# Optimization experiments

Hardware: AMD Instinct MI355X
Metric: run time of the kernel (lower is better)

The kernel has to match this reference:

```python
import jax, jax.numpy as jnp
import numpy as np
import math

B, T, C, H = 2, 2048, 1024, 16
HD = C // H

def setup_inputs() -> dict:
    key = jax.random.key(0)
    ks = jax.random.split(key, 5)
    s_in = 1.0 / math.sqrt(C)
    x = jax.random.normal(ks[0], (B, T, C), dtype=jnp.float32)
    W_attn = jax.random.normal(ks[1], (C, 3 * C), dtype=jnp.float32) * s_in
    b_attn = jnp.zeros((3 * C,), dtype=jnp.float32)
    W_proj = jax.random.normal(ks[2], (C, C), dtype=jnp.float32) * s_in
    b_proj = jnp.zeros((C,), dtype=jnp.float32)
    return {"x": x, "W_attn": W_attn, "b_attn": b_attn, "W_proj": W_proj, "b_proj": b_proj}

def reference(x, W_attn, b_attn, W_proj, b_proj):
    Bx, Tx, Cx = x.shape
    c = x @ W_attn + b_attn  # [B,T,3C]
    q, k, v = jnp.split(c, 3, axis=2)
    # [B,T,H,hd] -> [B,H,T,hd]
    q = q.reshape(Bx, Tx, H, HD).transpose(0, 2, 1, 3)
    k = k.reshape(Bx, Tx, H, HD).transpose(0, 2, 1, 3)
    v = v.reshape(Bx, Tx, H, HD).transpose(0, 2, 1, 3)
    # NOTE: module scales by 1/sqrt(C), not 1/sqrt(head_dim)
    attn = jnp.einsum('bhqd,bhkd->bhqk', q, k) * (1.0 / math.sqrt(Cx))
    causal = jnp.tril(jnp.ones((Tx, Tx), dtype=bool))
    attn = jnp.where(causal[None, None], attn, -jnp.inf)
    attn = jax.nn.softmax(attn, axis=-1)
    y = jnp.einsum('bhqk,bhkd->bhqd', attn, v)
    y = y.transpose(0, 2, 1, 3).reshape(Bx, Tx, Cx)
    return y @ W_proj + b_proj
```

## Files before the change

kernel.cpp:

```cpp
#include <hip/hip_runtime.h>
#include <math.h>

#define Bv 2
#define Tv 2048
#define Cv 1024
#define Hv 16
#define HDv 64
#define Mv (Bv * Tv)
#define SZv (Bv * Hv * Tv * HDv)

typedef short bf16x8 __attribute__((ext_vector_type(8)));
typedef float f32x4 __attribute__((ext_vector_type(4)));

static __device__ __forceinline__ unsigned short f2bf(float f) {
    unsigned u = __float_as_uint(f);
    u += 0x7fffu + ((u >> 16) & 1u);
    return (unsigned short)(u >> 16);
}

static __device__ __forceinline__ unsigned f2bf2(float a, float b) {
    unsigned r;
    asm("v_cvt_pk_bf16_f32 %0, %1, %2" : "=v"(r) : "v"(a), "v"(b));
    return r;
}

#define AS1 __attribute__((address_space(1)))
#define AS3 __attribute__((address_space(3)))
#define GLD16(gp, lp) __builtin_amdgcn_global_load_lds( \
    (AS1 const void*)(const void*)(gp), (AS3 void*)(void*)(lp), 16, 0, 0)

__global__ __launch_bounds__(256) void cvt_kernel(
    const float* __restrict__ src, unsigned short* __restrict__ dst, int n4)
{
    int i = blockIdx.x * 256 + threadIdx.x;
    if (i < n4) {
        float4 f = ((const float4*)src)[i];
        ushort4 u;
        u.x = f2bf(f.x); u.y = f2bf(f.y); u.z = f2bf(f.z); u.w = f2bf(f.w);
        ((ushort4*)dst)[i] = u;
    }
}

__global__ __launch_bounds__(256) void transpose_kernel(
    const float* __restrict__ src, unsigned short* __restrict__ dst,
    int R, int Ncols)
{
    __shared__ float tile[32][33];
    const int c0 = blockIdx.x * 32, r0 = blockIdx.y * 32;
    const int tx = threadIdx.x & 31, ty = threadIdx.x >> 5;
    #pragma unroll
    for (int i = 0; i < 4; ++i)
        tile[ty + i * 8][tx] = src[(size_t)(r0 + ty + i * 8) * Ncols + c0 + tx];
    __syncthreads();
    #pragma unroll
    for (int i = 0; i < 4; ++i)
        dst[(size_t)(c0 + ty + i * 8) * R + r0 + tx] = f2bf(tile[tx][ty + i * 8]);
}

__device__ __forceinline__ void mm_mainloop_1024(
    const unsigned short* __restrict__ A, const unsigned short* __restrict__ Bt,
    unsigned short* AsLds, unsigned short* BsLds,
    int rowBase, int colBase, f32x4 acc[4][4])
{
    const int tid  = threadIdx.x;
    const int lane = tid & 63;
    const int w    = tid >> 6;
    const int quad = lane >> 4, l15 = lane & 15;
    const int wm = (w >> 1) * 64, wn = (w & 1) * 64;
    const int K = 1024;

    const int g0 = (w * 2 + 0) * 64 + lane;
    const int g1 = (w * 2 + 1) * 64 + lane;
    const int r0 = g0 >> 2, r1 = g1 >> 2;
    const int kc0 = (g0 & 3) ^ ((r0 >> 1) & 3);
    const int kc1 = (g1 & 3) ^ ((r1 >> 1) & 3);
    const size_t offA0 = (size_t)(rowBase + r0) * K + kc0 * 8;
    const size_t offA1 = (size_t)(rowBase + r1) * K + kc1 * 8;
    const size_t offB0 = (size_t)(colBase + r0) * K + kc0 * 8;
    const size_t offB1 = (size_t)(colBase + r1) * K + kc1 * 8;
    unsigned short* ldsA0 = AsLds + (size_t)(w * 2 + 0) * 64 * 8;
    unsigned short* ldsA1 = AsLds + (size_t)(w * 2 + 1) * 64 * 8;
    unsigned short* ldsB0 = BsLds + (size_t)(w * 2 + 0) * 64 * 8;
    unsigned short* ldsB1 = BsLds + (size_t)(w * 2 + 1) * 64 * 8;

    const int sw = quad ^ ((l15 >> 1) & 3);
    int aoff[4], boff[4];
    #pragma unroll
    for (int i = 0; i < 4; ++i) {
        aoff[i] = ((wm + i * 16 + l15) * 4 + sw) * 8;
        boff[i] = ((wn + i * 16 + l15) * 4 + sw) * 8;
    }

    for (int k0 = 0; k0 < K; k0 += 32) {
        GLD16(A + offA0 + k0, ldsA0);
        GLD16(A + offA1 + k0, ldsA1);
        GLD16(Bt + offB0 + k0, ldsB0);
        GLD16(Bt + offB1 + k0, ldsB1);
        asm volatile("s_waitcnt vmcnt(0)" ::: "memory");
        __syncthreads();

        bf16x8 a[4], b[4];
        #pragma unroll
        for (int i = 0; i < 4; ++i) a[i] = *(const bf16x8*)(AsLds + aoff[i]);
        #pragma unroll
        for (int i = 0; i < 4; ++i) b[i] = *(const bf16x8*)(BsLds + boff[i]);

        #pragma unroll
        for (int mi = 0; mi < 4; ++mi)
            #pragma unroll
            for (int ni = 0; ni < 4; ++ni)
                acc[mi][ni] = __builtin_amdgcn_mfma_f32_16x16x32_bf16(
                    a[mi], b[ni], acc[mi][ni], 0, 0, 0);
        __syncthreads();
    }
}

__global__ __launch_bounds__(256) void qkv_mm_kernel(
    const unsigned short* __restrict__ xB, const unsigned short* __restrict__ WaT,
    const float* __restrict__ bias,
    unsigned short* __restrict__ qB, unsigned short* __restrict__ kB,
    unsigned short* __restrict__ vT)
{
    __shared__ __align__(16) unsigned short lds[128 * 136];
    const int rowBase = blockIdx.y * 128;
    const int colBase = blockIdx.x * 128;

    f32x4 acc[4][4];
    #pragma unroll
    for (int i = 0; i < 4; ++i)
        #pragma unroll
        for (int j = 0; j < 4; ++j) acc[i][j] = (f32x4){0.f, 0.f, 0.f, 0.f};

    mm_mainloop_1024(xB, WaT, lds, lds + 4096, rowBase, colBase, acc);

    const int tid = threadIdx.x, lane = tid & 63, w = tid >> 6;
    const int quad = lane >> 4, l15 = lane & 15;
    const int wm = (w >> 1) * 64, wn = (w & 1) * 64;
    const int s = colBase / Cv;
    const int tloc = rowBase & (Tv - 1);
    const int bh0 = (rowBase / Tv) * Hv + (colBase % Cv) / HDv;

    if (s < 2) {
        const float qs = (s == 0) ? 0.04508422f : 1.0f;
        #pragma unroll
        for (int mi = 0; mi < 4; ++mi)
            #pragma unroll
            for (int ni = 0; ni < 4; ++ni) {
                float bv = bias[colBase + wn + ni * 16 + l15];
                #pragma unroll
                for (int r = 0; r < 4; ++r) {
                    int m = wm + mi * 16 + quad * 4 + r;
                    int n = wn + ni * 16 + l15;
                    lds[m * 136 + n] = f2bf((acc[mi][ni][r] + bv) * qs);
                }
            }
        __syncthreads();
        unsigned short* dst = (s == 0) ? qB : kB;
        #pragma unroll
        for (int it = 0; it < 8; ++it) {
            int cc = tid + it * 256;
            int m = cc >> 4, j = cc & 15;
            uint4 v = *(const uint4*)(lds + m * 136 + j * 8);
            int hh = j >> 3, d0 = (j & 7) * 8;
            *(uint4*)(dst + ((size_t)(bh0 + hh) * Tv + tloc + m) * HDv + d0) = v;
        }
    } else {
        #pragma unroll
        for (int mi = 0; mi < 4; ++mi)
            #pragma unroll
            for (int ni = 0; ni < 4; ++ni) {
                float bv = bias[colBase + wn + ni * 16 + l15];
                #pragma unroll
                for (int r = 0; r < 4; ++r) {
                    int m = wm + mi * 16 + quad * 4 + r;
                    int n = wn + ni * 16 + l15;
                    lds[n * 136 + m] = f2bf(acc[mi][ni][r] + bv);
                }
            }
        __syncthreads();
        #pragma unroll
        for (int it = 0; it < 8; ++it) {
            int cc = tid + it * 256;
            int n = cc >> 4, j = cc & 15;
            uint4 v = *(const uint4*)(lds + n * 136 + j * 8);
            int hh = n >> 6, d = n & 63;
            *(uint4*)(vT + ((size_t)(bh0 + hh) * HDv + d) * Tv + tloc + j * 8) = v;
        }
    }
}

__global__ __launch_bounds__(256) void proj_mm_kernel(
    const unsigned short* __restrict__ y0B, const unsigned short* __restrict__ WpT,
    const float* __restrict__ bias, float* __restrict__ out)
{
    __shared__ __align__(16) unsigned short lds[8192];
    const int rowBase = blockIdx.y * 128;
    const int colBase = blockIdx.x * 128;

    f32x4 acc[4][4];
    #pragma unroll
    for (int i = 0; i < 4; ++i)
        #pragma unroll
        for (int j = 0; j < 4; ++j) acc[i][j] = (f32x4){0.f, 0.f, 0.f, 0.f};

    mm_mainloop_1024(y0B, WpT, lds, lds + 4096, rowBase, colBase, acc);

    const int tid = threadIdx.x, lane = tid & 63, w = tid >> 6;
    const int quad = lane >> 4, l15 = lane & 15;
    const int wm = (w >> 1) * 64, wn = (w & 1) * 64;

    #pragma unroll
    for (int mi = 0; mi < 4; ++mi)
        #pragma unroll
        for (int ni = 0; ni < 4; ++ni) {
            int n = colBase + wn + ni * 16 + l15;
            float bv = bias[n];
            #pragma unroll
            for (int r = 0; r < 4; ++r) {
                int m = rowBase + wm + mi * 16 + quad * 4 + r;
                out[(size_t)m * Cv + n] = acc[mi][ni][r] + bv;
            }
        }
}

__global__ __launch_bounds__(256) void attn_kernel(
    const unsigned short* __restrict__ qB, const unsigned short* __restrict__ kB,
    const unsigned short* __restrict__ vT, unsigned short* __restrict__ y0B)
{
    __shared__ __align__(16) unsigned short kv[1024 * 8];
    __shared__ __align__(16) unsigned short Pb[4][16 * 72];

    const int tid  = threadIdx.x;
    const int lane = tid & 63;
    const int w    = tid >> 6;
    const int quad = lane >> 4;
    const int l15  = lane & 15;

    const int qt = 31 - (blockIdx.x >> 5);
    const int bh = blockIdx.x & 31;
    const int qwbase = qt * 64 + w * 16;

    const unsigned short* qrow = qB + ((size_t)bh * Tv + qwbase + l15) * HDv;
    const bf16x8 Qa0 = *(const bf16x8*)(qrow + quad * 8);
    const bf16x8 Qa1 = *(const bf16x8*)(qrow + 32 + quad * 8);

    f32x4 O[4];
    float l[4] = {0.f, 0.f, 0.f, 0.f};
    #pragma unroll
    for (int n = 0; n < 4; ++n) O[n] = (f32x4){0.f, 0.f, 0.f, 0.f};

    const unsigned short* Kbase = kB + (size_t)bh * Tv * HDv;
    const unsigned short* Vbase = vT + (size_t)bh * HDv * Tv;
    unsigned short* Pw = &Pb[w][0];

    const unsigned short* gK[2];
    unsigned short* dK[2];
    #pragma unroll
    for (int i = 0; i < 2; ++i) {
        int slot = tid + i * 256;
        int row = slot >> 3;
        int g = (slot & 7) ^ ((row >> 2) & 7);
        gK[i] = Kbase + row * HDv + g * 8;
        dK[i] = kv + (size_t)(i * 256 + w * 64) * 8;
    }
    const unsigned short* gV[2];
    unsigned short* dV[2];
    #pragma unroll
    for (int i = 0; i < 2; ++i) {
        int slot = tid + i * 256;
        int d = slot >> 3;
        int g = (slot & 7) ^ (d & 7);
        gV[i] = Vbase + (size_t)d * Tv + g * 8;
        dV[i] = kv + (size_t)(512 + i * 256 + w * 64) * 8;
    }

    int koff[4][2], voff[4][2];
    #pragma unroll
    for (int ct = 0; ct < 4; ++ct) {
        int row = ct + 4 * l15;
        #pragma unroll
        for (int j = 0; j < 2; ++j)
            koff[ct][j] = (row * 8 + ((quad + 4 * j) ^ (l15 & 7))) * 8;
    }
    #pragma unroll
    for (int nt = 0; nt < 4; ++nt) {
        int d = nt * 16 + l15;
        #pragma unroll
        for (int j = 0; j < 2; ++j)
            voff[nt][j] = (512 + d) * 0 + (512 * 8) + (d * 8 + ((quad + 4 * j) ^ (l15 & 7))) * 8;
    }

    for (int kt = 0; kt <= qt; ++kt) {
        const int kbase = kt * 64;

        GLD16(gK[0] + kbase * HDv, dK[0]);
        GLD16(gK[1] + kbase * HDv, dK[1]);
        GLD16(gV[0] + kbase, dV[0]);
        GLD16(gV[1] + kbase, dV[1]);
        asm volatile("s_waitcnt vmcnt(0)" ::: "memory");
        __syncthreads();

        bf16x8 Kb[4][2], Vb[4][2];
        #pragma unroll
        for (int ct = 0; ct < 4; ++ct) {
            Kb[ct][0] = *(const bf16x8*)(kv + koff[ct][0]);
            Kb[ct][1] = *(const bf16x8*)(kv + koff[ct][1]);
        }
        #pragma unroll
        for (int nt = 0; nt < 4; ++nt) {
            Vb[nt][0] = *(const bf16x8*)(kv + voff[nt][0]);
            Vb[nt][1] = *(const bf16x8*)(kv + voff[nt][1]);
        }

        f32x4 S[4];
        #pragma unroll
        for (int ct = 0; ct < 4; ++ct) {
            S[ct] = (f32x4){0.f, 0.f, 0.f, 0.f};
            S[ct] = __builtin_amdgcn_mfma_f32_16x16x32_bf16(Qa0, Kb[ct][0], S[ct], 0, 0, 0);
            S[ct] = __builtin_amdgcn_mfma_f32_16x16x32_bf16(Qa1, Kb[ct][1], S[ct], 0, 0, 0);
        }

        if (kt == qt) {
            #pragma unroll
            for (int ct = 0; ct < 4; ++ct)
                #pragma unroll
                for (int r = 0; r < 4; ++r)
                    if (ct + 4 * l15 > w * 16 + quad * 4 + r) S[ct][r] = -1e30f;
        }

        float p[4][4];
        #pragma unroll
        for (int ct = 0; ct < 4; ++ct)
            #pragma unroll
            for (int r = 0; r < 4; ++r)
                p[ct][r] = __builtin_amdgcn_exp2f(S[ct][r]);
        #pragma unroll
        for (int r = 0; r < 4; ++r)
            l[r] += (p[0][r] + p[1][r]) + (p[2][r] + p[3][r]);

        #pragma unroll
        for (int r = 0; r < 4; ++r) {
            uint2 u = make_uint2(f2bf2(p[0][r], p[1][r]), f2bf2(p[2][r], p[3][r]));
            *(uint2*)(Pw + (quad * 4 + r) * 72 + l15 * 4) = u;
        }
        __asm__ volatile("s_waitcnt lgkmcnt(0)" ::: "memory");
        const bf16x8 Pa0 = *(const bf16x8*)(Pw + l15 * 72 + quad * 8);
        const bf16x8 Pa1 = *(const bf16x8*)(Pw + l15 * 72 + 32 + quad * 8);

        #pragma unroll
        for (int nt = 0; nt < 4; ++nt) {
            O[nt] = __builtin_amdgcn_mfma_f32_16x16x32_bf16(Pa0, Vb[nt][0], O[nt], 0, 0, 0);
            O[nt] = __builtin_amdgcn_mfma_f32_16x16x32_bf16(Pa1, Vb[nt][1], O[nt], 0, 0, 0);
        }
        __syncthreads();
    }

    #pragma unroll
    for (int r = 0; r < 4; ++r) {
        l[r] += __shfl_xor(l[r], 1);
        l[r] += __shfl_xor(l[r], 2);
        l[r] += __shfl_xor(l[r], 4);
        l[r] += __shfl_xor(l[r], 8);
    }

    const int b = bh >> 4, h = bh & 15;
    #pragma unroll
    for (int r = 0; r < 4; ++r) {
        float inv = 1.f / l[r];
        int q = qwbase + quad * 4 + r;
        unsigned short* dst = y0B + ((size_t)(b * Tv + q)) * Cv + h * HDv + l15;
        #pragma unroll
        for (int n = 0; n < 4; ++n) dst[n * 16] = f2bf(O[n][r] * inv);
    }
}

extern "C" void kernel_launch(void* const* d_in, const int* in_sizes, int n_in,
                              void* d_out, int out_size, void* d_ws, size_t ws_size,
                              hipStream_t stream) {
    const float* x      = (const float*)d_in[0];
    const float* W_attn = (const float*)d_in[1];
    const float* b_attn = (const float*)d_in[2];
    const float* W_proj = (const float*)d_in[3];
    const float* b_proj = (const float*)d_in[4];
    float* out = (float*)d_out;

    unsigned short* xB  = (unsigned short*)d_ws;
    unsigned short* WaT = xB  + (size_t)Mv * Cv;
    unsigned short* WpT = WaT + (size_t)3 * Cv * Cv;
    unsigned short* qB  = WpT + (size_t)Cv * Cv;
    unsigned short* kB  = qB + (size_t)SZv;
    unsigned short* vT  = kB + (size_t)SZv;
    unsigned short* y0B = vT + (size_t)SZv;

    dim3 blk(256);
    cvt_kernel<<<dim3((Mv * Cv / 4) / 256), blk, 0, stream>>>(x, xB, Mv * Cv / 4);
    transpose_kernel<<<dim3(3 * Cv / 32, Cv / 32), blk, 0, stream>>>(W_attn, WaT, Cv, 3 * Cv);
    transpose_kernel<<<dim3(Cv / 32, Cv / 32), blk, 0, stream>>>(W_proj, WpT, Cv, Cv);
    qkv_mm_kernel<<<dim3(3 * Cv / 128, Mv / 128), blk, 0, stream>>>(xB, WaT, b_attn, qB, kB, vT);
    attn_kernel<<<dim3(Bv * Hv * (Tv / 64)), blk, 0, stream>>>(qB, kB, vT, y0B);
    proj_mm_kernel<<<dim3(Cv / 128, Mv / 128), blk, 0, stream>>>(y0B, WpT, b_proj, out);
}
```

Baseline: 191.8 us.

## Double-buffer LDS tiles in GEMM mainloop and attention KV loop

Both the shared GEMM mainloop and the attention KV loop now prefetch the next tile into a second LDS buffer with async global-to-LDS loads while computing on the current one. They wait with a partial vmcnt, so only the current tile's loads must have arrived. This hides global memory latency behind MFMA work. In exchange it doubles LDS usage per block, which may reduce occupancy, and it relies on hand-placed s_waitcnt and s_barrier ordering.

```diff
diff --git a/kernel.cpp b/kernel.cpp
--- a/kernel.cpp
+++ b/kernel.cpp
@@ -29,6 +29,10 @@
 #define GLD16(gp, lp) __builtin_amdgcn_global_load_lds( \
     (AS1 const void*)(const void*)(gp), (AS3 void*)(void*)(lp), 16, 0, 0)
 
+#define WAITVM(n) asm volatile("s_waitcnt vmcnt(" #n ")" ::: "memory")
+#define WAITLGKM0 asm volatile("s_waitcnt lgkmcnt(0)" ::: "memory")
+#define BARRIER   asm volatile("s_barrier" ::: "memory")
+
 __global__ __launch_bounds__(256) void cvt_kernel(
     const float* __restrict__ src, unsigned short* __restrict__ dst, int n4)
 {
@@ -59,8 +63,7 @@
 
 __device__ __forceinline__ void mm_mainloop_1024(
     const unsigned short* __restrict__ A, const unsigned short* __restrict__ Bt,
-    unsigned short* AsLds, unsigned short* BsLds,
-    int rowBase, int colBase, f32x4 acc[4][4])
+    unsigned short* lds, int rowBase, int colBase, f32x4 acc[4][4])
 {
     const int tid  = threadIdx.x;
     const int lane = tid & 63;
@@ -78,32 +81,44 @@
     const size_t offA1 = (size_t)(rowBase + r1) * K + kc1 * 8;
     const size_t offB0 = (size_t)(colBase + r0) * K + kc0 * 8;
     const size_t offB1 = (size_t)(colBase + r1) * K + kc1 * 8;
-    unsigned short* ldsA0 = AsLds + (size_t)(w * 2 + 0) * 64 * 8;
-    unsigned short* ldsA1 = AsLds + (size_t)(w * 2 + 1) * 64 * 8;
-    unsigned short* ldsB0 = BsLds + (size_t)(w * 2 + 0) * 64 * 8;
-    unsigned short* ldsB1 = BsLds + (size_t)(w * 2 + 1) * 64 * 8;
+    unsigned short* ldsA0 = lds + (w * 2 + 0) * 512;
+    unsigned short* ldsA1 = lds + (w * 2 + 1) * 512;
+    unsigned short* ldsB0 = lds + 4096 + (w * 2 + 0) * 512;
+    unsigned short* ldsB1 = lds + 4096 + (w * 2 + 1) * 512;
 
     const int sw = quad ^ ((l15 >> 1) & 3);
     int aoff[4], boff[4];
     #pragma unroll
     for (int i = 0; i < 4; ++i) {
         aoff[i] = ((wm + i * 16 + l15) * 4 + sw) * 8;
-        boff[i] = ((wn + i * 16 + l15) * 4 + sw) * 8;
-    }
-
-    for (int k0 = 0; k0 < K; k0 += 32) {
-        GLD16(A + offA0 + k0, ldsA0);
-        GLD16(A + offA1 + k0, ldsA1);
-        GLD16(Bt + offB0 + k0, ldsB0);
-        GLD16(Bt + offB1 + k0, ldsB1);
-        asm volatile("s_waitcnt vmcnt(0)" ::: "memory");
-        __syncthreads();
+        boff[i] = 4096 + ((wn + i * 16 + l15) * 4 + sw) * 8;
+    }
+
+    GLD16(A + offA0, ldsA0);
+    GLD16(A + offA1, ldsA1);
+    GLD16(Bt + offB0, ldsB0);
+    GLD16(Bt + offB1, ldsB1);
+
+    for (int i = 0; i < 32; ++i) {
+        const int cur = (i & 1) * 8192;
+        const int nxt = 8192 - cur;
+        if (i < 31) {
+            const int k1 = (i + 1) * 32;
+            GLD16(A + offA0 + k1, ldsA0 + nxt);
+            GLD16(A + offA1 + k1, ldsA1 + nxt);
+            GLD16(Bt + offB0 + k1, ldsB0 + nxt);
+            GLD16(Bt + offB1 + k1, ldsB1 + nxt);
+            WAITVM(4);
+        } else {
+            WAITVM(0);
+        }
+        BARRIER;
 
         bf16x8 a[4], b[4];
         #pragma unroll
-        for (int i = 0; i < 4; ++i) a[i] = *(const bf16x8*)(AsLds + aoff[i]);
-        #pragma unroll
-        for (int i = 0; i < 4; ++i) b[i] = *(const bf16x8*)(BsLds + boff[i]);
+        for (int j = 0; j < 4; ++j) a[j] = *(const bf16x8*)(lds + cur + aoff[j]);
+        #pragma unroll
+        for (int j = 0; j < 4; ++j) b[j] = *(const bf16x8*)(lds + cur + boff[j]);
 
         #pragma unroll
         for (int mi = 0; mi < 4; ++mi)
@@ -111,7 +126,9 @@
             for (int ni = 0; ni < 4; ++ni)
                 acc[mi][ni] = __builtin_amdgcn_mfma_f32_16x16x32_bf16(
                     a[mi], b[ni], acc[mi][ni], 0, 0, 0);
-        __syncthreads();
+
+        WAITLGKM0;
+        BARRIER;
     }
 }
 
@@ -131,7 +148,8 @@
         #pragma unroll
         for (int j = 0; j < 4; ++j) acc[i][j] = (f32x4){0.f, 0.f, 0.f, 0.f};
 
-    mm_mainloop_1024(xB, WaT, lds, lds + 4096, rowBase, colBase, acc);
+    mm_mainloop_1024(xB, WaT, lds, rowBase, colBase, acc);
+    __syncthreads();
 
     const int tid = threadIdx.x, lane = tid & 63, w = tid >> 6;
     const int quad = lane >> 4, l15 = lane & 15;
@@ -193,7 +211,7 @@
     const unsigned short* __restrict__ y0B, const unsigned short* __restrict__ WpT,
     const float* __restrict__ bias, float* __restrict__ out)
 {
-    __shared__ __align__(16) unsigned short lds[8192];
+    __shared__ __align__(16) unsigned short lds[16384];
     const int rowBase = blockIdx.y * 128;
     const int colBase = blockIdx.x * 128;
 
@@ -203,7 +221,7 @@
         #pragma unroll
         for (int j = 0; j < 4; ++j) acc[i][j] = (f32x4){0.f, 0.f, 0.f, 0.f};
 
-    mm_mainloop_1024(y0B, WpT, lds, lds + 4096, rowBase, colBase, acc);
+    mm_mainloop_1024(y0B, WpT, lds, rowBase, colBase, acc);
 
     const int tid = threadIdx.x, lane = tid & 63, w = tid >> 6;
     const int quad = lane >> 4, l15 = lane & 15;
@@ -227,7 +245,7 @@
     const unsigned short* __restrict__ qB, const unsigned short* __restrict__ kB,
     const unsigned short* __restrict__ vT, unsigned short* __restrict__ y0B)
 {
-    __shared__ __align__(16) unsigned short kv[1024 * 8];
+    __shared__ __align__(16) unsigned short kv[2 * 8192];
     __shared__ __align__(16) unsigned short Pb[4][16 * 72];
 
     const int tid  = threadIdx.x;
@@ -243,6 +261,7 @@
     const unsigned short* qrow = qB + ((size_t)bh * Tv + qwbase + l15) * HDv;
     const bf16x8 Qa0 = *(const bf16x8*)(qrow + quad * 8);
     const bf16x8 Qa1 = *(const bf16x8*)(qrow + 32 + quad * 8);
+    WAITVM(0);
 
     f32x4 O[4];
     float l[4] = {0.f, 0.f, 0.f, 0.f};
@@ -253,25 +272,19 @@
     const unsigned short* Vbase = vT + (size_t)bh * HDv * Tv;
     unsigned short* Pw = &Pb[w][0];
 
-    const unsigned short* gK[2];
-    unsigned short* dK[2];
+    const unsigned short* gK[2]; unsigned short* dK[2];
+    const unsigned short* gV[2]; unsigned short* dV[2];
     #pragma unroll
     for (int i = 0; i < 2; ++i) {
         int slot = tid + i * 256;
         int row = slot >> 3;
-        int g = (slot & 7) ^ ((row >> 2) & 7);
-        gK[i] = Kbase + row * HDv + g * 8;
+        int gk = (slot & 7) ^ ((row >> 2) & 7);
+        gK[i] = Kbase + row * HDv + gk * 8;
         dK[i] = kv + (size_t)(i * 256 + w * 64) * 8;
-    }
-    const unsigned short* gV[2];
-    unsigned short* dV[2];
-    #pragma unroll
-    for (int i = 0; i < 2; ++i) {
-        int slot = tid + i * 256;
         int d = slot >> 3;
-        int g = (slot & 7) ^ (d & 7);
-        gV[i] = Vbase + (size_t)d * Tv + g * 8;
-        dV[i] = kv + (size_t)(512 + i * 256 + w * 64) * 8;
+        int gv = (slot & 7) ^ (d & 7);
+        gV[i] = Vbase + (size_t)d * Tv + gv * 8;
+        dV[i] = kv + 4096 + (size_t)(i * 256 + w * 64) * 8;
     }
 
     int koff[4][2], voff[4][2];
@@ -287,29 +300,39 @@
         int d = nt * 16 + l15;
         #pragma unroll
         for (int j = 0; j < 2; ++j)
-            voff[nt][j] = (512 + d) * 0 + (512 * 8) + (d * 8 + ((quad + 4 * j) ^ (l15 & 7))) * 8;
-    }
+            voff[nt][j] = 4096 + (d * 8 + ((quad + 4 * j) ^ (l15 & 7))) * 8;
+    }
+
+    GLD16(gK[0], dK[0]);
+    GLD16(gK[1], dK[1]);
+    GLD16(gV[0], dV[0]);
+    GLD16(gV[1], dV[1]);
 
     for (int kt = 0; kt <= qt; ++kt) {
-        const int kbase = kt * 64;
-
-        GLD16(gK[0] + kbase * HDv, dK[0]);
-        GLD16(gK[1] + kbase * HDv, dK[1]);
-        GLD16(gV[0] + kbase, dV[0]);
-        GLD16(gV[1] + kbase, dV[1]);
-        asm volatile("s_waitcnt vmcnt(0)" ::: "memory");
-        __syncthreads();
+        const int cur = (kt & 1) * 8192;
+        const int nxt = 8192 - cur;
+        if (kt < qt) {
+            const int kb1 = (kt + 1) * 64;
+            GLD16(gK[0] + (size_t)kb1 * HDv, dK[0] + nxt);
+            GLD16(gK[1] + (size_t)kb1 * HDv, dK[1] + nxt);
+            GLD16(gV[0] + kb1, dV[0] + nxt);
+            GLD16(gV[1] + kb1, dV[1] + nxt);
+            WAITVM(4);
+        } else {
+            WAITVM(0);
+        }
+        BARRIER;
 
         bf16x8 Kb[4][2], Vb[4][2];
         #pragma unroll
         for (int ct = 0; ct < 4; ++ct) {
-            Kb[ct][0] = *(const bf16x8*)(kv + koff[ct][0]);
-            Kb[ct][1] = *(const bf16x8*)(kv + koff[ct][1]);
+            Kb[ct][0] = *(const bf16x8*)(kv + cur + koff[ct][0]);
+            Kb[ct][1] = *(const bf16x8*)(kv + cur + koff[ct][1]);
         }
         #pragma unroll
         for (int nt = 0; nt < 4; ++nt) {
-            Vb[nt][0] = *(const bf16x8*)(kv + voff[nt][0]);
-            Vb[nt][1] = *(const bf16x8*)(kv + voff[nt][1]);
+            Vb[nt][0] = *(const bf16x8*)(kv + cur + voff[nt][0]);
+            Vb[nt][1] = *(const bf16x8*)(kv + cur + voff[nt][1]);
         }
 
         f32x4 S[4];
@@ -343,7 +366,7 @@
             uint2 u = make_uint2(f2bf2(p[0][r], p[1][r]), f2bf2(p[2][r], p[3][r]));
             *(uint2*)(Pw + (quad * 4 + r) * 72 + l15 * 4) = u;
         }
-        __asm__ volatile("s_waitcnt lgkmcnt(0)" ::: "memory");
+        WAITLGKM0;
         const bf16x8 Pa0 = *(const bf16x8*)(Pw + l15 * 72 + quad * 8);
         const bf16x8 Pa1 = *(const bf16x8*)(Pw + l15 * 72 + 32 + quad * 8);
 
@@ -352,7 +375,9 @@
             O[nt] = __builtin_amdgcn_mfma_f32_16x16x32_bf16(Pa0, Vb[nt][0], O[nt], 0, 0, 0);
             O[nt] = __builtin_amdgcn_mfma_f32_16x16x32_bf16(Pa1, Vb[nt][1], O[nt], 0, 0, 0);
         }
-        __syncthreads();
+
+        WAITLGKM0;
+        BARRIER;
     }
 
     #pragma unroll
```

Measured after the change: 181.8 us. -5.2%, faster.
